# Kernel tuning notes

Measured on AMD Instinct MI355X. Metric: run time of the kernel, lower is better.

Reference implementation:

```python
import jax, jax.numpy as jnp
import numpy as np
from itertools import product

N = 120000      # active voxels
D = 128         # dense grid resolution per axis
CIN = 64
COUT = 64
K = 27          # 3x3x3 kernel volume
EPS = 1e-5


def setup_inputs() -> dict:
    # Build a random sparse voxel set and its kernel-offset neighbor map (torchsparse kmap).
    rng = np.random.default_rng(0)
    flat = rng.choice(D ** 3, size=N, replace=False)
    cz, cy, cx = np.unravel_index(flat, (D, D, D))
    coords = np.stack([cz, cy, cx], axis=1)               # [N, 3]
    lut = np.full(D ** 3, -1, dtype=np.int64)
    lut[flat] = np.arange(N)
    nbr = np.empty((K, N), dtype=np.int32)
    for k, (dz, dy, dx) in enumerate(product((-1, 0, 1), repeat=3)):
        nc = coords + np.array([dz, dy, dx])
        valid = np.all((nc >= 0) & (nc < D), axis=1)
        fl = np.ravel_multi_index(np.clip(nc, 0, D - 1).T, (D, D, D))
        nbr[k] = np.where(valid, lut[fl], -1).astype(np.int32)

    key = jax.random.key(0)
    k1, k2, k3, k4 = jax.random.split(key, 4)
    feats = jax.random.normal(k1, (N, CIN), dtype=jnp.float32)
    # torchsparse Conv3d weight layout: [kernel_volume, in_channels, out_channels]
    weight = jax.random.normal(k2, (K, CIN, COUT), dtype=jnp.float32) / np.float32(np.sqrt(K * CIN))
    gamma = jax.random.uniform(k3, (COUT,), dtype=jnp.float32, minval=0.5, maxval=1.5)
    beta = jax.random.normal(k4, (COUT,), dtype=jnp.float32) * 0.1
    return {"feats": feats, "weight": weight, "gamma": gamma, "beta": beta,
            "neighbor_idx": jnp.asarray(nbr)}


def reference(feats, weight, gamma, beta, neighbor_idx):
    # Sparse conv = gather -> per-offset matmul -> accumulate (stride 1, same voxel set).
    mask = (neighbor_idx >= 0)                      # [K, N]
    safe = jnp.maximum(neighbor_idx, 0)
    gathered = feats[safe] * mask[..., None]        # [K, N, Cin], missing neighbors zeroed
    out = jnp.einsum('knc,kcd->nd', gathered, weight)  # [N, Cout]
    # BatchNorm over active voxels (training-mode batch statistics), then ReLU.
    mean = out.mean(axis=0)
    var = out.var(axis=0)
    y = gamma * (out - mean) * jax.lax.rsqrt(var + EPS) + beta
    return jnp.maximum(y, 0.0)
```

## Files before the change

### kernel.cpp

```cpp
#include <hip/hip_runtime.h>

#define NVOX 120000
#define KVOL 27
#define CH 64
#define TOTAL (NVOX * CH)
#define EPSV 1e-5f

typedef __attribute__((ext_vector_type(8))) short bf16x8;
typedef __attribute__((ext_vector_type(4))) float f32x4;
typedef __attribute__((ext_vector_type(4))) unsigned int u32x4;

__device__ __forceinline__ unsigned short f2bf(float f) {
    unsigned int u = __builtin_bit_cast(unsigned int, f);
    u += 0x7FFFu + ((u >> 16) & 1u);
    return (unsigned short)(u >> 16);
}

__global__ void prep(const float* __restrict__ w, unsigned short* __restrict__ wtf,
                     const float* __restrict__ f, unsigned short* __restrict__ fb,
                     float* __restrict__ stats) {
    const int b = blockIdx.x;
    const int tid = threadIdx.x;
    if (b < 432) {
        const int t = b * 256 + tid;
        const int d = t & 63, c = (t >> 6) & 63, k = t >> 12;
        const int grp = (d >> 4) * 2 + (c >> 5);
        const int l = ((c & 31) >> 3) * 16 + (d & 15);
        const int j = c & 7;
        wtf[(((size_t)k * 8 + grp) * 64 + l) * 8 + j] = f2bf(w[t]);
        if (b == 0 && tid < 128) stats[tid] = 0.f;
    } else {
        const int t = (b - 432) * 256 + tid;
        const float4 x = ((const float4*)f)[t];
        ushort4 y;
        y.x = f2bf(x.x); y.y = f2bf(x.y); y.z = f2bf(x.z); y.w = f2bf(x.w);
        ((ushort4*)fb)[t] = y;
    }
}

__device__ __forceinline__ void gatherRow(const unsigned short* __restrict__ fb,
                                          int idx, int q, bf16x8& a0, bf16x8& a1) {
    const int safe = idx < 0 ? 0 : idx;
    const unsigned short* row = fb + (size_t)safe * CH + q * 8;
    a0 = *(const bf16x8*)row;
    a1 = *(const bf16x8*)(row + 32);
    if (idx < 0) {
        a0 = (bf16x8)(short)0;
        a1 = (bf16x8)(short)0;
    }
}

__launch_bounds__(256, 4)
__global__ void conv_mfma(const unsigned short* __restrict__ featsB,
                          const unsigned short* __restrict__ WtF,
                          const int* __restrict__ nbr,
                          float* __restrict__ out,
                          float* __restrict__ stats) {
    __shared__ __align__(16) unsigned short ldsW[2][4096];
    __shared__ float lstats[128];
    const int tid = threadIdx.x;
    const int lane = tid & 63;
    const int wave = tid >> 6;
    const int m = lane & 15;
    const int q = lane >> 4;
    const int v0 = blockIdx.x * 64 + wave * 16;

    const int c0 = tid, c1 = tid + 256;

    u32x4 wr0 = *(const u32x4*)(WtF + (size_t)c0 * 8);
    u32x4 wr1 = *(const u32x4*)(WtF + (size_t)c1 * 8);
    *(u32x4*)(&ldsW[0][c0 * 8]) = wr0;
    *(u32x4*)(&ldsW[0][c1 * 8]) = wr1;
    wr0 = *(const u32x4*)(WtF + 4096 + (size_t)c0 * 8);
    wr1 = *(const u32x4*)(WtF + 4096 + (size_t)c1 * 8);

    bf16x8 a0, a1;
    gatherRow(featsB, nbr[v0 + m], q, a0, a1);
    int idx_nxt = nbr[NVOX + v0 + m];

    f32x4 acc[4];
#pragma unroll
    for (int nt = 0; nt < 4; ++nt) acc[nt] = (f32x4){0.f, 0.f, 0.f, 0.f};
    if (tid < 128) lstats[tid] = 0.f;
    __syncthreads();

    int bsel = 0;
    for (int k = 0; k < KVOL; ++k) {
        const unsigned short* bufR = &ldsW[bsel][0];
        unsigned short* bufW = &ldsW[bsel ^ 1][0];

        if (k + 1 < KVOL) {
            *(u32x4*)(bufW + c0 * 8) = wr0;
            *(u32x4*)(bufW + c1 * 8) = wr1;
        }
        if (k + 2 < KVOL) {
            wr0 = *(const u32x4*)(WtF + (size_t)(k + 2) * 4096 + c0 * 8);
            wr1 = *(const u32x4*)(WtF + (size_t)(k + 2) * 4096 + c1 * 8);
        }
        int idx_n2 = 0;
        if (k + 2 < KVOL) idx_n2 = nbr[(size_t)(k + 2) * NVOX + v0 + m];
        bf16x8 an0, an1;
        if (k + 1 < KVOL) gatherRow(featsB, idx_nxt, q, an0, an1);

#pragma unroll
        for (int nt = 0; nt < 4; ++nt) {
            const bf16x8 b0 = *(const bf16x8*)(bufR + (nt * 2 + 0) * 512 + lane * 8);
            const bf16x8 b1 = *(const bf16x8*)(bufR + (nt * 2 + 1) * 512 + lane * 8);
            acc[nt] = __builtin_amdgcn_mfma_f32_16x16x32_bf16(a0, b0, acc[nt], 0, 0, 0);
            acc[nt] = __builtin_amdgcn_mfma_f32_16x16x32_bf16(a1, b1, acc[nt], 0, 0, 0);
        }

        if (k + 1 < KVOL) {
            a0 = an0; a1 = an1;
            idx_nxt = idx_n2;
            bsel ^= 1;
            __syncthreads();
        }
    }

    float* ob = out + (size_t)(v0 + q * 4) * CH + m;
#pragma unroll
    for (int nt = 0; nt < 4; ++nt)
#pragma unroll
        for (int r = 0; r < 4; ++r)
            ob[(size_t)r * CH + nt * 16] = acc[nt][r];

#pragma unroll
    for (int nt = 0; nt < 4; ++nt) {
        float s = 0.f, s2 = 0.f;
#pragma unroll
        for (int r = 0; r < 4; ++r) {
            const float x = acc[nt][r];
            s += x;
            s2 = fmaf(x, x, s2);
        }
        s  += __shfl_xor(s, 16);  s  += __shfl_xor(s, 32);
        s2 += __shfl_xor(s2, 16); s2 += __shfl_xor(s2, 32);
        if (lane < 16) {
            atomicAdd(&lstats[nt * 16 + m], s);
            atomicAdd(&lstats[64 + nt * 16 + m], s2);
        }
    }
    __syncthreads();
    if (tid < 128) atomicAdd(&stats[tid], lstats[tid]);
}

__launch_bounds__(256)
__global__ void bn_relu(float* __restrict__ out, const float* __restrict__ stats,
                        const float* __restrict__ gamma, const float* __restrict__ beta) {
    __shared__ float sb[128];
    const int tid = threadIdx.x;
    if (tid < 64) {
        const float inv_n = 1.0f / (float)NVOX;
        const float mean = stats[tid] * inv_n;
        const float var = stats[64 + tid] * inv_n - mean * mean;
        const float sc = gamma[tid] * rsqrtf(var + EPSV);
        sb[tid] = sc;
        sb[64 + tid] = beta[tid] - mean * sc;
    }
    __syncthreads();
    const int e = blockIdx.x * 256 + tid;
    float4* o4 = (float4*)out;
    float4 x = o4[e];
    const int cb = (e & 15) * 4;
    x.x = fmaxf(fmaf(x.x, sb[cb + 0], sb[64 + cb + 0]), 0.f);
    x.y = fmaxf(fmaf(x.y, sb[cb + 1], sb[64 + cb + 1]), 0.f);
    x.z = fmaxf(fmaf(x.z, sb[cb + 2], sb[64 + cb + 2]), 0.f);
    x.w = fmaxf(fmaf(x.w, sb[cb + 3], sb[64 + cb + 3]), 0.f);
    o4[e] = x;
}

extern "C" void kernel_launch(void* const* d_in, const int* in_sizes, int n_in,
                              void* d_out, int out_size, void* d_ws, size_t ws_size,
                              hipStream_t stream) {
    const float* feats  = (const float*)d_in[0];
    const float* weight = (const float*)d_in[1];
    const float* gamma  = (const float*)d_in[2];
    const float* beta   = (const float*)d_in[3];
    const int*   nbr    = (const int*)d_in[4];
    float* out = (float*)d_out;

    float* stats = (float*)d_ws;
    unsigned short* WtF    = (unsigned short*)((char*)d_ws + 512);
    unsigned short* featsB = (unsigned short*)((char*)d_ws + 512 + 221184);

    prep<<<432 + TOTAL / 4 / 256, 256, 0, stream>>>(weight, WtF, feats, featsB, stats);
    conv_mfma<<<NVOX / 64, 256, 0, stream>>>(featsB, WtF, nbr, out, stats);
    bn_relu<<<TOTAL / 4 / 256, 256, 0, stream>>>(out, stats, gamma, beta);
}
```

Baseline: 176.2 us.

## Process kernel offsets in pairs per barrier and grid-stride prep/bn kernels

The conv main loop now handles two kernel offsets per iteration, using 16 KB weight slices per LDS buffer and a zero-padded 28th slice, so the number of __syncthreads barriers roughly halves and two feature gathers are in flight at once. The prep and bn_relu kernels switch to fixed grids with grid-stride loops to cut block launch overhead. This costs more LDS and registers per block, which may lower occupancy, and adds wasted MFMA work on the padded final offset.

```diff
diff --git a/kernel.cpp b/kernel.cpp
--- a/kernel.cpp
+++ b/kernel.cpp
@@ -4,7 +4,9 @@
 #define KVOL 27
 #define CH 64
 #define TOTAL (NVOX * CH)
+#define NF4 (TOTAL / 4)
 #define EPSV 1e-5f
+#define NPAIR 14
 
 typedef __attribute__((ext_vector_type(8))) short bf16x8;
 typedef __attribute__((ext_vector_type(4))) float f32x4;
@@ -29,12 +31,16 @@
         const int j = c & 7;
         wtf[(((size_t)k * 8 + grp) * 64 + l) * 8 + j] = f2bf(w[t]);
         if (b == 0 && tid < 128) stats[tid] = 0.f;
+    } else if (b < 436) {
+        const int t = (b - 432) * 256 + tid;
+        ((ushort4*)(wtf + 27 * 4096))[t] = (ushort4){0, 0, 0, 0};
     } else {
-        const int t = (b - 432) * 256 + tid;
-        const float4 x = ((const float4*)f)[t];
-        ushort4 y;
-        y.x = f2bf(x.x); y.y = f2bf(x.y); y.z = f2bf(x.z); y.w = f2bf(x.w);
-        ((ushort4*)fb)[t] = y;
+        for (int t = (b - 436) * 256 + tid; t < NF4; t += 1000 * 256) {
+            const float4 x = ((const float4*)f)[t];
+            ushort4 y;
+            y.x = f2bf(x.x); y.y = f2bf(x.y); y.z = f2bf(x.z); y.w = f2bf(x.w);
+            ((ushort4*)fb)[t] = y;
+        }
     }
 }
 
@@ -56,7 +62,7 @@
                           const int* __restrict__ nbr,
                           float* __restrict__ out,
                           float* __restrict__ stats) {
-    __shared__ __align__(16) unsigned short ldsW[2][4096];
+    __shared__ __align__(16) unsigned short ldsW[2][8192];
     __shared__ float lstats[128];
     const int tid = threadIdx.x;
     const int lane = tid & 63;
@@ -65,18 +71,28 @@
     const int q = lane >> 4;
     const int v0 = blockIdx.x * 64 + wave * 16;
 
-    const int c0 = tid, c1 = tid + 256;
-
-    u32x4 wr0 = *(const u32x4*)(WtF + (size_t)c0 * 8);
-    u32x4 wr1 = *(const u32x4*)(WtF + (size_t)c1 * 8);
-    *(u32x4*)(&ldsW[0][c0 * 8]) = wr0;
-    *(u32x4*)(&ldsW[0][c1 * 8]) = wr1;
-    wr0 = *(const u32x4*)(WtF + 4096 + (size_t)c0 * 8);
-    wr1 = *(const u32x4*)(WtF + 4096 + (size_t)c1 * 8);
-
-    bf16x8 a0, a1;
-    gatherRow(featsB, nbr[v0 + m], q, a0, a1);
-    int idx_nxt = nbr[NVOX + v0 + m];
+    const int o0 = tid * 8, o1 = (tid + 256) * 8, o2 = (tid + 512) * 8, o3 = (tid + 768) * 8;
+
+    {
+        u32x4 t0 = *(const u32x4*)(WtF + o0);
+        u32x4 t1 = *(const u32x4*)(WtF + o1);
+        u32x4 t2 = *(const u32x4*)(WtF + o2);
+        u32x4 t3 = *(const u32x4*)(WtF + o3);
+        *(u32x4*)(&ldsW[0][o0]) = t0;
+        *(u32x4*)(&ldsW[0][o1]) = t1;
+        *(u32x4*)(&ldsW[0][o2]) = t2;
+        *(u32x4*)(&ldsW[0][o3]) = t3;
+    }
+    u32x4 wr0 = *(const u32x4*)(WtF + 8192 + o0);
+    u32x4 wr1 = *(const u32x4*)(WtF + 8192 + o1);
+    u32x4 wr2 = *(const u32x4*)(WtF + 8192 + o2);
+    u32x4 wr3 = *(const u32x4*)(WtF + 8192 + o3);
+
+    bf16x8 a[2][2];
+    gatherRow(featsB, nbr[v0 + m], q, a[0][0], a[0][1]);
+    gatherRow(featsB, nbr[NVOX + v0 + m], q, a[1][0], a[1][1]);
+    int j0 = nbr[2 * NVOX + v0 + m];
+    int j1 = nbr[3 * NVOX + v0 + m];
 
     f32x4 acc[4];
 #pragma unroll
@@ -85,34 +101,53 @@
     __syncthreads();
 
     int bsel = 0;
-    for (int k = 0; k < KVOL; ++k) {
+    for (int p = 0; p < NPAIR; ++p) {
         const unsigned short* bufR = &ldsW[bsel][0];
         unsigned short* bufW = &ldsW[bsel ^ 1][0];
 
-        if (k + 1 < KVOL) {
-            *(u32x4*)(bufW + c0 * 8) = wr0;
-            *(u32x4*)(bufW + c1 * 8) = wr1;
-        }
-        if (k + 2 < KVOL) {
-            wr0 = *(const u32x4*)(WtF + (size_t)(k + 2) * 4096 + c0 * 8);
-            wr1 = *(const u32x4*)(WtF + (size_t)(k + 2) * 4096 + c1 * 8);
-        }
-        int idx_n2 = 0;
-        if (k + 2 < KVOL) idx_n2 = nbr[(size_t)(k + 2) * NVOX + v0 + m];
-        bf16x8 an0, an1;
-        if (k + 1 < KVOL) gatherRow(featsB, idx_nxt, q, an0, an1);
-
-#pragma unroll
-        for (int nt = 0; nt < 4; ++nt) {
-            const bf16x8 b0 = *(const bf16x8*)(bufR + (nt * 2 + 0) * 512 + lane * 8);
-            const bf16x8 b1 = *(const bf16x8*)(bufR + (nt * 2 + 1) * 512 + lane * 8);
-            acc[nt] = __builtin_amdgcn_mfma_f32_16x16x32_bf16(a0, b0, acc[nt], 0, 0, 0);
-            acc[nt] = __builtin_amdgcn_mfma_f32_16x16x32_bf16(a1, b1, acc[nt], 0, 0, 0);
-        }
-
-        if (k + 1 < KVOL) {
-            a0 = an0; a1 = an1;
-            idx_nxt = idx_n2;
+        if (p + 1 < NPAIR) {
+            *(u32x4*)(bufW + o0) = wr0;
+            *(u32x4*)(bufW + o1) = wr1;
+            *(u32x4*)(bufW + o2) = wr2;
+            *(u32x4*)(bufW + o3) = wr3;
+        }
+        if (p + 2 < NPAIR) {
+            const unsigned short* wp = WtF + (size_t)(p + 2) * 8192;
+            wr0 = *(const u32x4*)(wp + o0);
+            wr1 = *(const u32x4*)(wp + o1);
+            wr2 = *(const u32x4*)(wp + o2);
+            wr3 = *(const u32x4*)(wp + o3);
+        }
+        int n0 = -1, n1 = -1;
+        if (p + 2 < NPAIR) {
+            n0 = nbr[(size_t)(2 * p + 4) * NVOX + v0 + m];
+            n1 = (2 * p + 5 < KVOL) ? nbr[(size_t)(2 * p + 5) * NVOX + v0 + m] : -1;
+        }
+        bf16x8 an[2][2];
+        if (p + 1 < NPAIR) {
+            gatherRow(featsB, j0, q, an[0][0], an[0][1]);
+            gatherRow(featsB, j1, q, an[1][0], an[1][1]);
+        }
+
+#pragma unroll
+        for (int s = 0; s < 2; ++s) {
+            const unsigned short* base = bufR + s * 4096;
+#pragma unroll
+            for (int nt = 0; nt < 4; ++nt) {
+                const bf16x8 b0 = *(const bf16x8*)(base + (nt * 2 + 0) * 512 + lane * 8);
+                const bf16x8 b1 = *(const bf16x8*)(base + (nt * 2 + 1) * 512 + lane * 8);
+                acc[nt] = __builtin_amdgcn_mfma_f32_16x16x32_bf16(a[s][0], b0, acc[nt], 0, 0, 0);
+                acc[nt] = __builtin_amdgcn_mfma_f32_16x16x32_bf16(a[s][1], b1, acc[nt], 0, 0, 0);
+            }
+        }
+
+        if (p + 1 < NPAIR) {
+#pragma unroll
+            for (int s = 0; s < 2; ++s) {
+                a[s][0] = an[s][0];
+                a[s][1] = an[s][1];
+            }
+            j0 = n0; j1 = n1;
             bsel ^= 1;
             __syncthreads();
         }
@@ -159,15 +194,16 @@
         sb[64 + tid] = beta[tid] - mean * sc;
     }
     __syncthreads();
-    const int e = blockIdx.x * 256 + tid;
     float4* o4 = (float4*)out;
-    float4 x = o4[e];
-    const int cb = (e & 15) * 4;
-    x.x = fmaxf(fmaf(x.x, sb[cb + 0], sb[64 + cb + 0]), 0.f);
-    x.y = fmaxf(fmaf(x.y, sb[cb + 1], sb[64 + cb + 1]), 0.f);
-    x.z = fmaxf(fmaf(x.z, sb[cb + 2], sb[64 + cb + 2]), 0.f);
-    x.w = fmaxf(fmaf(x.w, sb[cb + 3], sb[64 + cb + 3]), 0.f);
-    o4[e] = x;
+    for (int e = blockIdx.x * 256 + tid; e < NF4; e += 960 * 256) {
+        float4 x = o4[e];
+        const int cb = (e & 15) * 4;
+        x.x = fmaxf(fmaf(x.x, sb[cb + 0], sb[64 + cb + 0]), 0.f);
+        x.y = fmaxf(fmaf(x.y, sb[cb + 1], sb[64 + cb + 1]), 0.f);
+        x.z = fmaxf(fmaf(x.z, sb[cb + 2], sb[64 + cb + 2]), 0.f);
+        x.w = fmaxf(fmaf(x.w, sb[cb + 3], sb[64 + cb + 3]), 0.f);
+        o4[e] = x;
+    }
 }
 
 extern "C" void kernel_launch(void* const* d_in, const int* in_sizes, int n_in,
@@ -182,9 +218,9 @@
 
     float* stats = (float*)d_ws;
     unsigned short* WtF    = (unsigned short*)((char*)d_ws + 512);
-    unsigned short* featsB = (unsigned short*)((char*)d_ws + 512 + 221184);
-
-    prep<<<432 + TOTAL / 4 / 256, 256, 0, stream>>>(weight, WtF, feats, featsB, stats);
+    unsigned short* featsB = (unsigned short*)((char*)d_ws + 512 + 229376);
+
+    prep<<<436 + 1000, 256, 0, stream>>>(weight, WtF, feats, featsB, stats);
     conv_mfma<<<NVOX / 64, 256, 0, stream>>>(featsB, WtF, nbr, out, stats);
-    bn_relu<<<TOTAL / 4 / 256, 256, 0, stream>>>(out, stats, gamma, beta);
-}
+    bn_relu<<<960, 256, 0, stream>>>(out, stats, gamma, beta);
+}
```

Measured after the change: 167.1 us. 5.2% less time.

## Drop LDS weight staging, tile 32 voxels per wave, skip empty offsets

Applied to the files above, without the earlier changes.

The conv kernel stops double-buffering weights through LDS with per-offset barriers. Each wave now reads weight fragments straight from global/L2, handles two 16-row tiles so each weight load feeds twice the MFMAs, and uses a ballot to skip gathers and MFMAs for offsets where no voxel in the tile has a neighbor. This halves the block count, adds bounds checks for the tail, and removes the software prefetch of the next gather, which may expose gather latency. Prep and bn_relu switch to grid-stride loops over fixed grid sizes.

```diff
diff --git a/kernel.cpp b/kernel.cpp
--- a/kernel.cpp
+++ b/kernel.cpp
@@ -4,11 +4,11 @@
 #define KVOL 27
 #define CH 64
 #define TOTAL (NVOX * CH)
+#define NF4 (TOTAL / 4)
 #define EPSV 1e-5f
 
 typedef __attribute__((ext_vector_type(8))) short bf16x8;
 typedef __attribute__((ext_vector_type(4))) float f32x4;
-typedef __attribute__((ext_vector_type(4))) unsigned int u32x4;
 
 __device__ __forceinline__ unsigned short f2bf(float f) {
     unsigned int u = __builtin_bit_cast(unsigned int, f);
@@ -30,11 +30,12 @@
         wtf[(((size_t)k * 8 + grp) * 64 + l) * 8 + j] = f2bf(w[t]);
         if (b == 0 && tid < 128) stats[tid] = 0.f;
     } else {
-        const int t = (b - 432) * 256 + tid;
-        const float4 x = ((const float4*)f)[t];
-        ushort4 y;
-        y.x = f2bf(x.x); y.y = f2bf(x.y); y.z = f2bf(x.z); y.w = f2bf(x.w);
-        ((ushort4*)fb)[t] = y;
+        for (int t = (b - 432) * 256 + tid; t < NF4; t += 1000 * 256) {
+            const float4 x = ((const float4*)f)[t];
+            ushort4 y;
+            y.x = f2bf(x.x); y.y = f2bf(x.y); y.z = f2bf(x.z); y.w = f2bf(x.w);
+            ((ushort4*)fb)[t] = y;
+        }
     }
 }
 
@@ -56,84 +57,93 @@
                           const int* __restrict__ nbr,
                           float* __restrict__ out,
                           float* __restrict__ stats) {
-    __shared__ __align__(16) unsigned short ldsW[2][4096];
     __shared__ float lstats[128];
     const int tid = threadIdx.x;
     const int lane = tid & 63;
     const int wave = tid >> 6;
     const int m = lane & 15;
     const int q = lane >> 4;
-    const int v0 = blockIdx.x * 64 + wave * 16;
-
-    const int c0 = tid, c1 = tid + 256;
-
-    u32x4 wr0 = *(const u32x4*)(WtF + (size_t)c0 * 8);
-    u32x4 wr1 = *(const u32x4*)(WtF + (size_t)c1 * 8);
-    *(u32x4*)(&ldsW[0][c0 * 8]) = wr0;
-    *(u32x4*)(&ldsW[0][c1 * 8]) = wr1;
-    wr0 = *(const u32x4*)(WtF + 4096 + (size_t)c0 * 8);
-    wr1 = *(const u32x4*)(WtF + 4096 + (size_t)c1 * 8);
-
-    bf16x8 a0, a1;
-    gatherRow(featsB, nbr[v0 + m], q, a0, a1);
-    int idx_nxt = nbr[NVOX + v0 + m];
-
-    f32x4 acc[4];
-#pragma unroll
-    for (int nt = 0; nt < 4; ++nt) acc[nt] = (f32x4){0.f, 0.f, 0.f, 0.f};
+    const int v0 = blockIdx.x * 128 + wave * 32;
+    const int r0 = v0 + m;
+    const int r1 = v0 + 16 + m;
+    const bool ok0 = r0 < NVOX;
+    const bool ok1 = r1 < NVOX;
+
+    f32x4 acc[2][4];
+#pragma unroll
+    for (int t = 0; t < 2; ++t)
+#pragma unroll
+        for (int nt = 0; nt < 4; ++nt)
+            acc[t][nt] = (f32x4){0.f, 0.f, 0.f, 0.f};
     if (tid < 128) lstats[tid] = 0.f;
     __syncthreads();
 
-    int bsel = 0;
+    int i0 = ok0 ? nbr[r0] : -1;
+    int i1 = ok1 ? nbr[r1] : -1;
+
     for (int k = 0; k < KVOL; ++k) {
-        const unsigned short* bufR = &ldsW[bsel][0];
-        unsigned short* bufW = &ldsW[bsel ^ 1][0];
-
+        const unsigned long long t0m = __ballot(i0 >= 0);
+        const unsigned long long t1m = __ballot(i1 >= 0);
+
+        bf16x8 a00, a01, a10, a11;
+        if (t0m) gatherRow(featsB, i0, q, a00, a01);
+        if (t1m) gatherRow(featsB, i1, q, a10, a11);
+
+        int i0n = -1, i1n = -1;
         if (k + 1 < KVOL) {
-            *(u32x4*)(bufW + c0 * 8) = wr0;
-            *(u32x4*)(bufW + c1 * 8) = wr1;
-        }
-        if (k + 2 < KVOL) {
-            wr0 = *(const u32x4*)(WtF + (size_t)(k + 2) * 4096 + c0 * 8);
-            wr1 = *(const u32x4*)(WtF + (size_t)(k + 2) * 4096 + c1 * 8);
-        }
-        int idx_n2 = 0;
-        if (k + 2 < KVOL) idx_n2 = nbr[(size_t)(k + 2) * NVOX + v0 + m];
-        bf16x8 an0, an1;
-        if (k + 1 < KVOL) gatherRow(featsB, idx_nxt, q, an0, an1);
-
-#pragma unroll
-        for (int nt = 0; nt < 4; ++nt) {
-            const bf16x8 b0 = *(const bf16x8*)(bufR + (nt * 2 + 0) * 512 + lane * 8);
-            const bf16x8 b1 = *(const bf16x8*)(bufR + (nt * 2 + 1) * 512 + lane * 8);
-            acc[nt] = __builtin_amdgcn_mfma_f32_16x16x32_bf16(a0, b0, acc[nt], 0, 0, 0);
-            acc[nt] = __builtin_amdgcn_mfma_f32_16x16x32_bf16(a1, b1, acc[nt], 0, 0, 0);
-        }
-
-        if (k + 1 < KVOL) {
-            a0 = an0; a1 = an1;
-            idx_nxt = idx_n2;
-            bsel ^= 1;
-            __syncthreads();
-        }
-    }
-
-    float* ob = out + (size_t)(v0 + q * 4) * CH + m;
-#pragma unroll
-    for (int nt = 0; nt < 4; ++nt)
-#pragma unroll
-        for (int r = 0; r < 4; ++r)
-            ob[(size_t)r * CH + nt * 16] = acc[nt][r];
+            const int* nb = nbr + (size_t)(k + 1) * NVOX;
+            i0n = ok0 ? nb[r0] : -1;
+            i1n = ok1 ? nb[r1] : -1;
+        }
+
+        if (t0m | t1m) {
+            const unsigned short* wk = WtF + (size_t)k * 4096 + lane * 8;
+            bf16x8 bfr[8];
+#pragma unroll
+            for (int h = 0; h < 8; ++h)
+                bfr[h] = *(const bf16x8*)(wk + h * 512);
+            if (t0m) {
+#pragma unroll
+                for (int nt = 0; nt < 4; ++nt) {
+                    acc[0][nt] = __builtin_amdgcn_mfma_f32_16x16x32_bf16(a00, bfr[nt * 2 + 0], acc[0][nt], 0, 0, 0);
+                    acc[0][nt] = __builtin_amdgcn_mfma_f32_16x16x32_bf16(a01, bfr[nt * 2 + 1], acc[0][nt], 0, 0, 0);
+                }
+            }
+            if (t1m) {
+#pragma unroll
+                for (int nt = 0; nt < 4; ++nt) {
+                    acc[1][nt] = __builtin_amdgcn_mfma_f32_16x16x32_bf16(a10, bfr[nt * 2 + 0], acc[1][nt], 0, 0, 0);
+                    acc[1][nt] = __builtin_amdgcn_mfma_f32_16x16x32_bf16(a11, bfr[nt * 2 + 1], acc[1][nt], 0, 0, 0);
+                }
+            }
+        }
+        i0 = i0n;
+        i1 = i1n;
+    }
+
+#pragma unroll
+    for (int t = 0; t < 2; ++t) {
+        const int rbase = v0 + t * 16 + q * 4;
+        float* ob = out + (size_t)rbase * CH + m;
+#pragma unroll
+        for (int nt = 0; nt < 4; ++nt)
+#pragma unroll
+            for (int r = 0; r < 4; ++r)
+                if (rbase + r < NVOX)
+                    ob[(size_t)r * CH + nt * 16] = acc[t][nt][r];
+    }
 
 #pragma unroll
     for (int nt = 0; nt < 4; ++nt) {
         float s = 0.f, s2 = 0.f;
 #pragma unroll
-        for (int r = 0; r < 4; ++r) {
-            const float x = acc[nt][r];
-            s += x;
-            s2 = fmaf(x, x, s2);
-        }
+        for (int t = 0; t < 2; ++t)
+#pragma unroll
+            for (int r = 0; r < 4; ++r) {
+                const float x = acc[t][nt][r];
+                s += x;
+                s2 = fmaf(x, x, s2);
+            }
         s  += __shfl_xor(s, 16);  s  += __shfl_xor(s, 32);
         s2 += __shfl_xor(s2, 16); s2 += __shfl_xor(s2, 32);
         if (lane < 16) {
@@ -159,15 +169,16 @@
         sb[64 + tid] = beta[tid] - mean * sc;
     }
     __syncthreads();
-    const int e = blockIdx.x * 256 + tid;
     float4* o4 = (float4*)out;
-    float4 x = o4[e];
-    const int cb = (e & 15) * 4;
-    x.x = fmaxf(fmaf(x.x, sb[cb + 0], sb[64 + cb + 0]), 0.f);
-    x.y = fmaxf(fmaf(x.y, sb[cb + 1], sb[64 + cb + 1]), 0.f);
-    x.z = fmaxf(fmaf(x.z, sb[cb + 2], sb[64 + cb + 2]), 0.f);
-    x.w = fmaxf(fmaf(x.w, sb[cb + 3], sb[64 + cb + 3]), 0.f);
-    o4[e] = x;
+    for (int e = blockIdx.x * 256 + tid; e < NF4; e += 960 * 256) {
+        float4 x = o4[e];
+        const int cb = (e & 15) * 4;
+        x.x = fmaxf(fmaf(x.x, sb[cb + 0], sb[64 + cb + 0]), 0.f);
+        x.y = fmaxf(fmaf(x.y, sb[cb + 1], sb[64 + cb + 1]), 0.f);
+        x.z = fmaxf(fmaf(x.z, sb[cb + 2], sb[64 + cb + 2]), 0.f);
+        x.w = fmaxf(fmaf(x.w, sb[cb + 3], sb[64 + cb + 3]), 0.f);
+        o4[e] = x;
+    }
 }
 
 extern "C" void kernel_launch(void* const* d_in, const int* in_sizes, int n_in,
@@ -184,7 +195,7 @@
     unsigned short* WtF    = (unsigned short*)((char*)d_ws + 512);
     unsigned short* featsB = (unsigned short*)((char*)d_ws + 512 + 221184);
 
-    prep<<<432 + TOTAL / 4 / 256, 256, 0, stream>>>(weight, WtF, feats, featsB, stats);
-    conv_mfma<<<NVOX / 64, 256, 0, stream>>>(featsB, WtF, nbr, out, stats);
-    bn_relu<<<TOTAL / 4 / 256, 256, 0, stream>>>(out, stats, gamma, beta);
-}
+    prep<<<432 + 1000, 256, 0, stream>>>(weight, WtF, feats, featsB, stats);
+    conv_mfma<<<(NVOX + 127) / 128, 256, 0, stream>>>(featsB, WtF, nbr, out, stats);
+    bn_relu<<<960, 256, 0, stream>>>(out, stats, gamma, beta);
+}
```

After: 156.5 us. 11.2% less time.
